# Performance work log

Measured on AMD Instinct MI355X. Metric: run time of the kernel, lower is better.

The kernel has to match this reference:

```python
import jax, jax.numpy as jnp
import numpy as np

DIM = 256
HEADS = 4
B, N = 2, 4096
NEG = -1e9
EPS = 1e-5


def setup_inputs() -> dict:
    key = jax.random.key(0)
    ks = jax.random.split(key, 12)
    s = 0.02
    inp = {
        "x": jax.random.normal(ks[0], (B, N, DIM), dtype=jnp.float32),
        "adj": jax.random.randint(ks[1], (B, N, N), 0, 2, dtype=jnp.int32),
        "Wq": jax.random.normal(ks[2], (DIM, DIM), dtype=jnp.float32) * s,
        "bq": jnp.zeros((DIM,), jnp.float32),
        "Wk": jax.random.normal(ks[3], (DIM, DIM), dtype=jnp.float32) * s,
        "bk": jnp.zeros((DIM,), jnp.float32),
        "Wv": jax.random.normal(ks[4], (DIM, DIM), dtype=jnp.float32) * s,
        "bv": jnp.zeros((DIM,), jnp.float32),
        "Wo": jax.random.normal(ks[5], (DIM, DIM), dtype=jnp.float32) * s,
        "bo": jnp.zeros((DIM,), jnp.float32),
        "gamma": jnp.ones((DIM,), jnp.float32),
        "beta": jnp.zeros((DIM,), jnp.float32),
    }
    return inp


def reference(x, adj, Wq, bq, Wk, bk, Wv, bv, Wo, bo, gamma, beta):
    Bx, Nx, C = x.shape
    H = HEADS
    D = C // H
    scale = D ** (-0.5)
    # torch Linear: y = x @ W.T + b
    def proj(W, b):
        return (x @ W.T + b).reshape(Bx, Nx, H, D).transpose(0, 2, 1, 3)  # [B,H,N,D]
    q = proj(Wq, bq)
    k = proj(Wk, bk)
    v = proj(Wv, bv)
    attn = jnp.einsum("bhnd,bhmd->bhnm", q, k) * scale          # [B,H,N,N]
    attn = jnp.where(adj[:, None, :, :] == 0, NEG, attn)
    attn = jax.nn.softmax(attn, axis=-1)
    # dropout omitted (eval mode / deterministic reference)
    out = jnp.einsum("bhnm,bhmd->bhnd", attn, v)                # [B,H,N,D]
    out = out.transpose(0, 2, 1, 3).reshape(Bx, Nx, C)
    out = out @ Wo.T + bo
    mu = jnp.mean(out, axis=-1, keepdims=True)
    var = jnp.var(out, axis=-1, keepdims=True)
    return (out - mu) * jax.lax.rsqrt(var + EPS) * gamma + beta
```

## Files before the change

### kernel.cpp

```cpp
#include <hip/hip_runtime.h>
#include <stdint.h>

#define CDIM 256
#define HEADS 4
#define HD 64
#define NB 2
#define NN 4096

typedef unsigned short u16;
typedef unsigned long long u64;
typedef __attribute__((ext_vector_type(8))) short short8;
typedef __attribute__((ext_vector_type(4))) float f32x4;

__device__ __forceinline__ void load8f(const float* p, float* f) {
  float4 a = reinterpret_cast<const float4*>(p)[0];
  float4 b = reinterpret_cast<const float4*>(p)[1];
  f[0] = a.x; f[1] = a.y; f[2] = a.z; f[3] = a.w;
  f[4] = b.x; f[5] = b.y; f[6] = b.z; f[7] = b.w;
}

__device__ __forceinline__ u16 f2bf(float f) {
  union { float f; unsigned u; } v; v.f = f;
  return (u16)((v.u + 0x7fffu + ((v.u >> 16) & 1u)) >> 16);
}

__global__ __launch_bounds__(256) void conv_bf16(
    const float* __restrict__ x,
    const float* __restrict__ Wq, const float* __restrict__ Wk,
    const float* __restrict__ Wv, const float* __restrict__ Wo,
    u16* __restrict__ xb, u16* __restrict__ Wqb, u16* __restrict__ Wkb,
    u16* __restrict__ Wvb, u16* __restrict__ Wob) {
  size_t base = ((size_t)blockIdx.x * 256 + threadIdx.x) * 8;
  const float* src;
  u16* dst;
  if (base < 2097152) {
    src = x + base; dst = xb + base;
  } else {
    size_t o = base - 2097152;
    int w = (int)(o >> 16);
    size_t lo = o & 65535;
    if (w == 0)      { src = Wq + lo; dst = Wqb + lo; }
    else if (w == 1) { src = Wk + lo; dst = Wkb + lo; }
    else if (w == 2) { src = Wv + lo; dst = Wvb + lo; }
    else             { src = Wo + lo; dst = Wob + lo; }
  }
  float f[8];
  load8f(src, f);
  short8 h;
#pragma unroll
  for (int i = 0; i < 8; ++i) h[i] = (short)f2bf(f[i]);
  *reinterpret_cast<short8*>(dst) = h;
}

__global__ __launch_bounds__(256) void adj_bits(const int* __restrict__ adj,
                                                u64* __restrict__ bm) {
  const int wave = threadIdx.x >> 6, lane = threadIdx.x & 63;
  const size_t widx = (size_t)blockIdx.x * 4 + wave;
  const size_t base = widx * 512;
#pragma unroll
  for (int it = 0; it < 8; ++it) {
    int a = adj[base + it * 64 + lane];
    u64 m = __ballot(a != 0);
    if (lane == 0) bm[widx * 8 + it] = m;
  }
}

__global__ __launch_bounds__(256) void qkv_gemm(
    const u16* __restrict__ xb,
    const u16* __restrict__ Wqb, const u16* __restrict__ Wkb,
    const u16* __restrict__ Wvb,
    const float* __restrict__ bq, const float* __restrict__ bk,
    const float* __restrict__ bv,
    u16* __restrict__ Qb, u16* __restrict__ Kb, u16* __restrict__ Vtb) {
  const int tid = threadIdx.x, w = tid >> 6, lane = tid & 63;
  const int quad = lane >> 4, l15 = lane & 15;
  const int tok0 = blockIdx.x * 16;
  const int b = tok0 >> 12, nl = tok0 & 4095;
  const int ym = blockIdx.y;

  f32x4 acc[4];
#pragma unroll
  for (int i = 0; i < 4; ++i) acc[i] = (f32x4){0.f, 0.f, 0.f, 0.f};

  if (ym < 2) {
    const u16* Wb = (ym == 0) ? Wqb : Wkb;
    const float* bias = (ym == 0) ? bq : bk;
    const float scale = (ym == 0) ? 0.125f : 1.0f;
    u16* outp = (ym == 0) ? Qb : Kb;
#pragma unroll
    for (int ks = 0; ks < 8; ++ks) {
      short8 af = *reinterpret_cast<const short8*>(
          &xb[(size_t)(tok0 + l15) * 256 + ks * 32 + quad * 8]);
#pragma unroll
      for (int ns = 0; ns < 4; ++ns) {
        short8 bf = *reinterpret_cast<const short8*>(
            &Wb[(size_t)(w * 64 + ns * 16 + l15) * 256 + ks * 32 + quad * 8]);
        acc[ns] = __builtin_amdgcn_mfma_f32_16x16x32_bf16(af, bf, acc[ns], 0, 0, 0);
      }
    }
#pragma unroll
    for (int ns = 0; ns < 4; ++ns) {
      int d = ns * 16 + l15;
      float bb = bias[w * 64 + d];
#pragma unroll
      for (int r = 0; r < 4; ++r) {
        int tok = nl + quad * 4 + r;
        outp[((size_t)(b * HEADS + w) * NN + tok) * HD + d] =
            f2bf((acc[ns][r] + bb) * scale);
      }
    }
  } else {
#pragma unroll
    for (int ks = 0; ks < 8; ++ks) {
      short8 xf = *reinterpret_cast<const short8*>(
          &xb[(size_t)(tok0 + l15) * 256 + ks * 32 + quad * 8]);
#pragma unroll
      for (int ms = 0; ms < 4; ++ms) {
        short8 wf = *reinterpret_cast<const short8*>(
            &Wvb[(size_t)(w * 64 + ms * 16 + l15) * 256 + ks * 32 + quad * 8]);
        acc[ms] = __builtin_amdgcn_mfma_f32_16x16x32_bf16(wf, xf, acc[ms], 0, 0, 0);
      }
    }
#pragma unroll
    for (int ms = 0; ms < 4; ++ms) {
#pragma unroll
      for (int r = 0; r < 4; ++r) {
        int d = ms * 16 + quad * 4 + r;
        float bb = bv[w * 64 + d];
        Vtb[((size_t)((b * HEADS + w) * HD + d)) * NN + nl + l15] =
            f2bf(acc[ms][r] + bb);
      }
    }
  }
}

__global__ __launch_bounds__(256) void attn_mfma(
    const u16* __restrict__ Qb, const u16* __restrict__ Kb,
    const u16* __restrict__ Vtb, const u64* __restrict__ bm,
    u16* __restrict__ Ab) {
  __shared__ u16 Ks[2][64 * 72];
  __shared__ u16 Vs[2][64 * 72];
  __shared__ u16 Ps[4][16 * 72];

  const int tid = threadIdx.x;
  const int wave = tid >> 6, lane = tid & 63;
  const int quad = lane >> 4, l15 = lane & 15;
  const int bh = blockIdx.y, b = bh >> 2, h = bh & 3;
  const int q0 = blockIdx.x * 64 + wave * 16;

  const u16* qr = Qb + ((size_t)bh * NN + q0 + l15) * HD + quad * 8;
  const short8 qf0 = *reinterpret_cast<const short8*>(qr);
  const short8 qf1 = *reinterpret_cast<const short8*>(qr + 32);

  f32x4 Oacc[4];
#pragma unroll
  for (int i = 0; i < 4; ++i) Oacc[i] = (f32x4){0.f, 0.f, 0.f, 0.f};
  float li[4] = {0.f, 0.f, 0.f, 0.f};
  const f32x4 z4 = {0.f, 0.f, 0.f, 0.f};
  u16* Pw = &Ps[wave][0];
  const u64* bmr = bm + ((size_t)b * NN + q0 + quad * 4) * 64;

  const u16* kbase = Kb + (size_t)bh * NN * HD;
  const u16* vbase = Vtb + (size_t)bh * HD * NN;
  const int c0 = tid, c1 = tid + 256;
  const int r0 = c0 >> 3, o0 = (c0 & 7) * 8;
  const int r1 = c1 >> 3, o1 = (c1 & 7) * 8;

  uint4 kreg0, kreg1, vreg0, vreg1;
  kreg0 = *reinterpret_cast<const uint4*>(kbase + (size_t)r0 * HD + o0);
  kreg1 = *reinterpret_cast<const uint4*>(kbase + (size_t)r1 * HD + o1);
  vreg0 = *reinterpret_cast<const uint4*>(vbase + (size_t)r0 * NN + o0);
  vreg1 = *reinterpret_cast<const uint4*>(vbase + (size_t)r1 * NN + o1);
  *reinterpret_cast<uint4*>(&Ks[0][r0 * 72 + o0]) = kreg0;
  *reinterpret_cast<uint4*>(&Ks[0][r1 * 72 + o1]) = kreg1;
  *reinterpret_cast<uint4*>(&Vs[0][r0 * 72 + o0]) = vreg0;
  *reinterpret_cast<uint4*>(&Vs[0][r1 * 72 + o1]) = vreg1;
  __syncthreads();

  for (int mt = 0; mt < 64; ++mt) {
    const int m0 = mt * 64;
    const int buf = mt & 1;
    if (mt + 1 < 64) {
      const int mn = m0 + 64;
      kreg0 = *reinterpret_cast<const uint4*>(kbase + (size_t)(mn + r0) * HD + o0);
      kreg1 = *reinterpret_cast<const uint4*>(kbase + (size_t)(mn + r1) * HD + o1);
      vreg0 = *reinterpret_cast<const uint4*>(vbase + (size_t)r0 * NN + mn + o0);
      vreg1 = *reinterpret_cast<const uint4*>(vbase + (size_t)r1 * NN + mn + o1);
    }

    u64 am[4];
#pragma unroll
    for (int r = 0; r < 4; ++r) am[r] = bmr[r * 64 + mt];

#pragma unroll
    for (int t = 0; t < 4; ++t) {
      const u16* kr = &Ks[buf][(t * 16 + l15) * 72 + quad * 8];
      short8 kf0 = *reinterpret_cast<const short8*>(kr);
      short8 kf1 = *reinterpret_cast<const short8*>(kr + 32);
      f32x4 s = __builtin_amdgcn_mfma_f32_16x16x32_bf16(qf0, kf0, z4, 0, 0, 0);
      s = __builtin_amdgcn_mfma_f32_16x16x32_bf16(qf1, kf1, s, 0, 0, 0);
      const int sh = t * 16 + l15;
#pragma unroll
      for (int r = 0; r < 4; ++r) {
        float p = ((unsigned)(am[r] >> sh) & 1u) ? __expf(s[r]) : 0.f;
        li[r] += p;
        Pw[(quad * 4 + r) * 72 + sh] = f2bf(p);
      }
    }
    __asm__ volatile("s_waitcnt lgkmcnt(0)" ::: "memory");

    const short8 pf0 = *reinterpret_cast<const short8*>(&Pw[l15 * 72 + quad * 8]);
    const short8 pf1 = *reinterpret_cast<const short8*>(&Pw[l15 * 72 + 32 + quad * 8]);
#pragma unroll
    for (int dt = 0; dt < 4; ++dt) {
      const u16* vr = &Vs[buf][(dt * 16 + l15) * 72 + quad * 8];
      short8 vf0 = *reinterpret_cast<const short8*>(vr);
      short8 vf1 = *reinterpret_cast<const short8*>(vr + 32);
      Oacc[dt] = __builtin_amdgcn_mfma_f32_16x16x32_bf16(pf0, vf0, Oacc[dt], 0, 0, 0);
      Oacc[dt] = __builtin_amdgcn_mfma_f32_16x16x32_bf16(pf1, vf1, Oacc[dt], 0, 0, 0);
    }

    if (mt + 1 < 64) {
      const int nb = (mt + 1) & 1;
      *reinterpret_cast<uint4*>(&Ks[nb][r0 * 72 + o0]) = kreg0;
      *reinterpret_cast<uint4*>(&Ks[nb][r1 * 72 + o1]) = kreg1;
      *reinterpret_cast<uint4*>(&Vs[nb][r0 * 72 + o0]) = vreg0;
      *reinterpret_cast<uint4*>(&Vs[nb][r1 * 72 + o1]) = vreg1;
    }
    __syncthreads();
  }

  float inv[4];
#pragma unroll
  for (int r = 0; r < 4; ++r) {
    float lt = li[r];
#pragma unroll
    for (int off = 1; off < 16; off <<= 1) lt += __shfl_xor(lt, off, 64);
    inv[r] = (lt > 0.f) ? (1.f / lt) : 0.f;
  }
#pragma unroll
  for (int r = 0; r < 4; ++r) {
    int tok = q0 + quad * 4 + r;
#pragma unroll
    for (int dt = 0; dt < 4; ++dt) {
      Ab[((size_t)b * NN + tok) * CDIM + h * HD + dt * 16 + l15] =
          f2bf(Oacc[dt][r] * inv[r]);
    }
  }
}

__global__ __launch_bounds__(256) void oproj_ln(
    const u16* __restrict__ Ab, const u16* __restrict__ Wob,
    const float* __restrict__ bo, const float* __restrict__ gamma,
    const float* __restrict__ beta, float* __restrict__ out) {
  __shared__ float ys[16][264];
  const int tid = threadIdx.x, w = tid >> 6, lane = tid & 63;
  const int quad = lane >> 4, l15 = lane & 15;
  const int tok0 = blockIdx.x * 16;

  f32x4 acc[4];
#pragma unroll
  for (int i = 0; i < 4; ++i) acc[i] = (f32x4){0.f, 0.f, 0.f, 0.f};

#pragma unroll
  for (int ks = 0; ks < 8; ++ks) {
    short8 af = *reinterpret_cast<const short8*>(
        &Ab[(size_t)(tok0 + l15) * 256 + ks * 32 + quad * 8]);
#pragma unroll
    for (int ns = 0; ns < 4; ++ns) {
      short8 bf = *reinterpret_cast<const short8*>(
          &Wob[(size_t)(w * 64 + ns * 16 + l15) * 256 + ks * 32 + quad * 8]);
      acc[ns] = __builtin_amdgcn_mfma_f32_16x16x32_bf16(af, bf, acc[ns], 0, 0, 0);
    }
  }

#pragma unroll
  for (int ns = 0; ns < 4; ++ns) {
    int ch = w * 64 + ns * 16 + l15;
    float bb = bo[ch];
#pragma unroll
    for (int r = 0; r < 4; ++r) ys[quad * 4 + r][ch] = acc[ns][r] + bb;
  }
  __syncthreads();

  float g[4], bt[4];
#pragma unroll
  for (int i = 0; i < 4; ++i) {
    g[i] = gamma[lane + i * 64];
    bt[i] = beta[lane + i * 64];
  }
#pragma unroll
  for (int rr = 0; rr < 4; ++rr) {
    int r = w * 4 + rr;
    float v[4], s = 0.f, s2 = 0.f;
#pragma unroll
    for (int i = 0; i < 4; ++i) {
      v[i] = ys[r][lane + i * 64];
      s += v[i];
      s2 = fmaf(v[i], v[i], s2);
    }
#pragma unroll
    for (int off = 32; off > 0; off >>= 1) {
      s += __shfl_xor(s, off, 64);
      s2 += __shfl_xor(s2, off, 64);
    }
    float mu = s * (1.f / 256.f);
    float rs = rsqrtf(s2 * (1.f / 256.f) - mu * mu + 1e-5f);
    float* orow = out + (size_t)(tok0 + r) * 256;
#pragma unroll
    for (int i = 0; i < 4; ++i)
      orow[lane + i * 64] = (v[i] - mu) * rs * g[i] + bt[i];
  }
}

extern "C" void kernel_launch(void* const* d_in, const int* in_sizes, int n_in,
                              void* d_out, int out_size, void* d_ws, size_t ws_size,
                              hipStream_t stream) {
  const float* x     = (const float*)d_in[0];
  const int*   adj   = (const int*)d_in[1];
  const float* Wq    = (const float*)d_in[2];
  const float* bq    = (const float*)d_in[3];
  const float* Wk    = (const float*)d_in[4];
  const float* bk    = (const float*)d_in[5];
  const float* Wv    = (const float*)d_in[6];
  const float* bv    = (const float*)d_in[7];
  const float* Wo    = (const float*)d_in[8];
  const float* bo    = (const float*)d_in[9];
  const float* gamma = (const float*)d_in[10];
  const float* beta  = (const float*)d_in[11];
  float* out = (float*)d_out;

  const size_t PER = (size_t)NB * HEADS * NN * HD;
  u16* xb  = (u16*)d_ws;
  u16* Wqb = xb + 2097152;
  u16* Wkb = Wqb + 65536;
  u16* Wvb = Wkb + 65536;
  u16* Wob = Wvb + 65536;
  u64* bmp = (u64*)(Wob + 65536);
  u16* Qb  = (u16*)(bmp + 524288);
  u16* Kb  = Qb + PER;
  u16* Vtb = Kb + PER;
  u16* Ab  = Vtb + PER;

  const size_t NEED = (size_t)((Ab + PER) - (u16*)d_ws) * sizeof(u16);
  if (ws_size < NEED) return;

  conv_bf16<<<dim3(1152), dim3(256), 0, stream>>>(
      x, Wq, Wk, Wv, Wo, xb, Wqb, Wkb, Wvb, Wob);

  adj_bits<<<dim3(16384), dim3(256), 0, stream>>>(adj, bmp);

  qkv_gemm<<<dim3(512, 3), dim3(256), 0, stream>>>(
      xb, Wqb, Wkb, Wvb, bq, bk, bv, Qb, Kb, Vtb);

  attn_mfma<<<dim3(NN / 64, NB * HEADS), dim3(256), 0, stream>>>(
      Qb, Kb, Vtb, bmp, Ab);

  oproj_ln<<<dim3((NB * NN) / 16), dim3(256), 0, stream>>>(
      Ab, Wob, bo, gamma, beta, out);
}
```

Measured before the change: 360.9 us.

## Split attention keys across two blocks, fuse prep kernels and x conversion

The attention kernel now splits the key range into two halves along a new grid dimension, doubling the block count from 512. Each half writes unnormalized bf16 partial outputs and row sums, which a new combine kernel merges before the output projection and layernorm. The adjacency bitmask and weight conversion are fused into one prep kernel, and x is converted to bf16 inside the QKV GEMM, removing a launch and an intermediate buffer. Q is prescaled by log2(e) so exp2f replaces __expf, and the K/V staging is simplified to a single shared buffer with two barriers per tile, trading overlap and extra partial-output traffic for more parallelism.

```diff
diff --git a/kernel.cpp b/kernel.cpp
--- a/kernel.cpp
+++ b/kernel.cpp
@@ -12,61 +12,67 @@
 typedef __attribute__((ext_vector_type(8))) short short8;
 typedef __attribute__((ext_vector_type(4))) float f32x4;
 
-__device__ __forceinline__ void load8f(const float* p, float* f) {
-  float4 a = reinterpret_cast<const float4*>(p)[0];
-  float4 b = reinterpret_cast<const float4*>(p)[1];
-  f[0] = a.x; f[1] = a.y; f[2] = a.z; f[3] = a.w;
-  f[4] = b.x; f[5] = b.y; f[6] = b.z; f[7] = b.w;
-}
+#define QSCALE 0.1803368801111244f
 
 __device__ __forceinline__ u16 f2bf(float f) {
   union { float f; unsigned u; } v; v.f = f;
   return (u16)((v.u + 0x7fffu + ((v.u >> 16) & 1u)) >> 16);
 }
-
-__global__ __launch_bounds__(256) void conv_bf16(
-    const float* __restrict__ x,
+__device__ __forceinline__ float bf2f(u16 u) {
+  union { unsigned u; float f; } v; v.u = ((unsigned)u) << 16; return v.f;
+}
+
+__global__ __launch_bounds__(256) void prep(
+    const int* __restrict__ adj, u64* __restrict__ bm,
     const float* __restrict__ Wq, const float* __restrict__ Wk,
     const float* __restrict__ Wv, const float* __restrict__ Wo,
-    u16* __restrict__ xb, u16* __restrict__ Wqb, u16* __restrict__ Wkb,
+    u16* __restrict__ Wqb, u16* __restrict__ Wkb,
     u16* __restrict__ Wvb, u16* __restrict__ Wob) {
-  size_t base = ((size_t)blockIdx.x * 256 + threadIdx.x) * 8;
-  const float* src;
-  u16* dst;
-  if (base < 2097152) {
-    src = x + base; dst = xb + base;
+  if (blockIdx.x < 16384) {
+    const int wave = threadIdx.x >> 6, lane = threadIdx.x & 63;
+    const size_t widx = (size_t)blockIdx.x * 4 + wave;
+    const size_t base = widx * 512;
+#pragma unroll
+    for (int it = 0; it < 8; ++it) {
+      int a = adj[base + it * 64 + lane];
+      u64 m = __ballot(a != 0);
+      if (lane == 0) bm[widx * 8 + it] = m;
+    }
   } else {
-    size_t o = base - 2097152;
-    int w = (int)(o >> 16);
-    size_t lo = o & 65535;
+    int bi = blockIdx.x - 16384;
+    size_t base = ((size_t)bi * 256 + threadIdx.x) * 8;
+    int w = (int)(base >> 16);
+    size_t lo = base & 65535;
+    const float* src;
+    u16* dst;
     if (w == 0)      { src = Wq + lo; dst = Wqb + lo; }
     else if (w == 1) { src = Wk + lo; dst = Wkb + lo; }
     else if (w == 2) { src = Wv + lo; dst = Wvb + lo; }
     else             { src = Wo + lo; dst = Wob + lo; }
-  }
-  float f[8];
-  load8f(src, f);
+    float4 a = reinterpret_cast<const float4*>(src)[0];
+    float4 b = reinterpret_cast<const float4*>(src)[1];
+    short8 h;
+    h[0] = (short)f2bf(a.x); h[1] = (short)f2bf(a.y);
+    h[2] = (short)f2bf(a.z); h[3] = (short)f2bf(a.w);
+    h[4] = (short)f2bf(b.x); h[5] = (short)f2bf(b.y);
+    h[6] = (short)f2bf(b.z); h[7] = (short)f2bf(b.w);
+    *reinterpret_cast<short8*>(dst) = h;
+  }
+}
+
+__device__ __forceinline__ short8 fragf32(const float* p) {
+  float4 a = reinterpret_cast<const float4*>(p)[0];
+  float4 b = reinterpret_cast<const float4*>(p)[1];
   short8 h;
-#pragma unroll
-  for (int i = 0; i < 8; ++i) h[i] = (short)f2bf(f[i]);
-  *reinterpret_cast<short8*>(dst) = h;
-}
-
-__global__ __launch_bounds__(256) void adj_bits(const int* __restrict__ adj,
-                                                u64* __restrict__ bm) {
-  const int wave = threadIdx.x >> 6, lane = threadIdx.x & 63;
-  const size_t widx = (size_t)blockIdx.x * 4 + wave;
-  const size_t base = widx * 512;
-#pragma unroll
-  for (int it = 0; it < 8; ++it) {
-    int a = adj[base + it * 64 + lane];
-    u64 m = __ballot(a != 0);
-    if (lane == 0) bm[widx * 8 + it] = m;
-  }
+  h[0] = (short)f2bf(a.x); h[1] = (short)f2bf(a.y);
+  h[2] = (short)f2bf(a.z); h[3] = (short)f2bf(a.w);
+  h[4] = (short)f2bf(b.x); h[5] = (short)f2bf(b.y);
+  h[6] = (short)f2bf(b.z); h[7] = (short)f2bf(b.w);
+  return h;
 }
 
 __global__ __launch_bounds__(256) void qkv_gemm(
-    const u16* __restrict__ xb,
+    const float* __restrict__ x,
     const u16* __restrict__ Wqb, const u16* __restrict__ Wkb,
     const u16* __restrict__ Wvb,
     const float* __restrict__ bq, const float* __restrict__ bk,
@@ -85,12 +91,11 @@
   if (ym < 2) {
     const u16* Wb = (ym == 0) ? Wqb : Wkb;
     const float* bias = (ym == 0) ? bq : bk;
-    const float scale = (ym == 0) ? 0.125f : 1.0f;
+    const float scale = (ym == 0) ? QSCALE : 1.0f;
     u16* outp = (ym == 0) ? Qb : Kb;
 #pragma unroll
     for (int ks = 0; ks < 8; ++ks) {
-      short8 af = *reinterpret_cast<const short8*>(
-          &xb[(size_t)(tok0 + l15) * 256 + ks * 32 + quad * 8]);
+      short8 af = fragf32(x + (size_t)(tok0 + l15) * 256 + ks * 32 + quad * 8);
 #pragma unroll
       for (int ns = 0; ns < 4; ++ns) {
         short8 bf = *reinterpret_cast<const short8*>(
@@ -112,8 +117,7 @@
   } else {
 #pragma unroll
     for (int ks = 0; ks < 8; ++ks) {
-      short8 xf = *reinterpret_cast<const short8*>(
-          &xb[(size_t)(tok0 + l15) * 256 + ks * 32 + quad * 8]);
+      short8 xf = fragf32(x + (size_t)(tok0 + l15) * 256 + ks * 32 + quad * 8);
 #pragma unroll
       for (int ms = 0; ms < 4; ++ms) {
         short8 wf = *reinterpret_cast<const short8*>(
@@ -137,9 +141,9 @@
 __global__ __launch_bounds__(256) void attn_mfma(
     const u16* __restrict__ Qb, const u16* __restrict__ Kb,
     const u16* __restrict__ Vtb, const u64* __restrict__ bm,
-    u16* __restrict__ Ab) {
-  __shared__ u16 Ks[2][64 * 72];
-  __shared__ u16 Vs[2][64 * 72];
+    u16* __restrict__ Opb, float* __restrict__ Lp) {
+  __shared__ u16 Ks[64 * 72];
+  __shared__ u16 Vs[64 * 72];
   __shared__ u16 Ps[4][16 * 72];
 
   const int tid = threadIdx.x;
@@ -147,6 +151,8 @@
   const int quad = lane >> 4, l15 = lane & 15;
   const int bh = blockIdx.y, b = bh >> 2, h = bh & 3;
   const int q0 = blockIdx.x * 64 + wave * 16;
+  const int half = blockIdx.z;
+  const int key0 = half * 2048;
 
   const u16* qr = Qb + ((size_t)bh * NN + q0 + l15) * HD + quad * 8;
   const short8 qf0 = *reinterpret_cast<const short8*>(qr);
@@ -158,34 +164,32 @@
   float li[4] = {0.f, 0.f, 0.f, 0.f};
   const f32x4 z4 = {0.f, 0.f, 0.f, 0.f};
   u16* Pw = &Ps[wave][0];
-  const u64* bmr = bm + ((size_t)b * NN + q0 + quad * 4) * 64;
+  const u64* bmr = bm + ((size_t)b * NN + q0 + quad * 4) * 64 + half * 32;
 
   const u16* kbase = Kb + (size_t)bh * NN * HD;
   const u16* vbase = Vtb + (size_t)bh * HD * NN;
-  const int c0 = tid, c1 = tid + 256;
-  const int r0 = c0 >> 3, o0 = (c0 & 7) * 8;
-  const int r1 = c1 >> 3, o1 = (c1 & 7) * 8;
-
-  uint4 kreg0, kreg1, vreg0, vreg1;
-  kreg0 = *reinterpret_cast<const uint4*>(kbase + (size_t)r0 * HD + o0);
-  kreg1 = *reinterpret_cast<const uint4*>(kbase + (size_t)r1 * HD + o1);
-  vreg0 = *reinterpret_cast<const uint4*>(vbase + (size_t)r0 * NN + o0);
-  vreg1 = *reinterpret_cast<const uint4*>(vbase + (size_t)r1 * NN + o1);
-  *reinterpret_cast<uint4*>(&Ks[0][r0 * 72 + o0]) = kreg0;
-  *reinterpret_cast<uint4*>(&Ks[0][r1 * 72 + o1]) = kreg1;
-  *reinterpret_cast<uint4*>(&Vs[0][r0 * 72 + o0]) = vreg0;
-  *reinterpret_cast<uint4*>(&Vs[0][r1 * 72 + o1]) = vreg1;
-  __syncthreads();
-
-  for (int mt = 0; mt < 64; ++mt) {
-    const int m0 = mt * 64;
-    const int buf = mt & 1;
-    if (mt + 1 < 64) {
-      const int mn = m0 + 64;
-      kreg0 = *reinterpret_cast<const uint4*>(kbase + (size_t)(mn + r0) * HD + o0);
-      kreg1 = *reinterpret_cast<const uint4*>(kbase + (size_t)(mn + r1) * HD + o1);
-      vreg0 = *reinterpret_cast<const uint4*>(vbase + (size_t)r0 * NN + mn + o0);
-      vreg1 = *reinterpret_cast<const uint4*>(vbase + (size_t)r1 * NN + mn + o1);
+  const int rr = tid >> 3, cc8 = (tid & 7) * 8;
+  const int rr2 = rr + 32;
+
+  uint4 k0, k1, v0, v1;
+  k0 = *reinterpret_cast<const uint4*>(kbase + (size_t)(key0 + rr) * HD + cc8);
+  k1 = *reinterpret_cast<const uint4*>(kbase + (size_t)(key0 + rr2) * HD + cc8);
+  v0 = *reinterpret_cast<const uint4*>(vbase + (size_t)rr * NN + key0 + cc8);
+  v1 = *reinterpret_cast<const uint4*>(vbase + (size_t)rr2 * NN + key0 + cc8);
+
+  for (int mt = 0; mt < 32; ++mt) {
+    __syncthreads();
+    *reinterpret_cast<uint4*>(&Ks[rr * 72 + cc8]) = k0;
+    *reinterpret_cast<uint4*>(&Ks[rr2 * 72 + cc8]) = k1;
+    *reinterpret_cast<uint4*>(&Vs[rr * 72 + cc8]) = v0;
+    *reinterpret_cast<uint4*>(&Vs[rr2 * 72 + cc8]) = v1;
+    __syncthreads();
+    if (mt + 1 < 32) {
+      int kb2 = key0 + (mt + 1) * 64;
+      k0 = *reinterpret_cast<const uint4*>(kbase + (size_t)(kb2 + rr) * HD + cc8);
+      k1 = *reinterpret_cast<const uint4*>(kbase + (size_t)(kb2 + rr2) * HD + cc8);
+      v0 = *reinterpret_cast<const uint4*>(vbase + (size_t)rr * NN + kb2 + cc8);
+      v1 = *reinterpret_cast<const uint4*>(vbase + (size_t)rr2 * NN + kb2 + cc8);
     }
 
     u64 am[4];
@@ -194,7 +198,7 @@
 
 #pragma unroll
     for (int t = 0; t < 4; ++t) {
-      const u16* kr = &Ks[buf][(t * 16 + l15) * 72 + quad * 8];
+      const u16* kr = &Ks[(t * 16 + l15) * 72 + quad * 8];
       short8 kf0 = *reinterpret_cast<const short8*>(kr);
       short8 kf1 = *reinterpret_cast<const short8*>(kr + 32);
       f32x4 s = __builtin_amdgcn_mfma_f32_16x16x32_bf16(qf0, kf0, z4, 0, 0, 0);
@@ -202,9 +206,9 @@
       const int sh = t * 16 + l15;
 #pragma unroll
       for (int r = 0; r < 4; ++r) {
-        float p = ((unsigned)(am[r] >> sh) & 1u) ? __expf(s[r]) : 0.f;
+        float p = ((unsigned)(am[r] >> sh) & 1u) ? exp2f(s[r]) : 0.f;
         li[r] += p;
-        Pw[(quad * 4 + r) * 72 + sh] = f2bf(p);
+        Pw[(quad * 4 + r) * 72 + sh] = (u16)(__float_as_uint(p) >> 16);
       }
     }
     __asm__ volatile("s_waitcnt lgkmcnt(0)" ::: "memory");
@@ -213,59 +217,80 @@
     const short8 pf1 = *reinterpret_cast<const short8*>(&Pw[l15 * 72 + 32 + quad * 8]);
 #pragma unroll
     for (int dt = 0; dt < 4; ++dt) {
-      const u16* vr = &Vs[buf][(dt * 16 + l15) * 72 + quad * 8];
+      const u16* vr = &Vs[(dt * 16 + l15) * 72 + quad * 8];
       short8 vf0 = *reinterpret_cast<const short8*>(vr);
       short8 vf1 = *reinterpret_cast<const short8*>(vr + 32);
       Oacc[dt] = __builtin_amdgcn_mfma_f32_16x16x32_bf16(pf0, vf0, Oacc[dt], 0, 0, 0);
       Oacc[dt] = __builtin_amdgcn_mfma_f32_16x16x32_bf16(pf1, vf1, Oacc[dt], 0, 0, 0);
     }
-
-    if (mt + 1 < 64) {
-      const int nb = (mt + 1) & 1;
-      *reinterpret_cast<uint4*>(&Ks[nb][r0 * 72 + o0]) = kreg0;
-      *reinterpret_cast<uint4*>(&Ks[nb][r1 * 72 + o1]) = kreg1;
-      *reinterpret_cast<uint4*>(&Vs[nb][r0 * 72 + o0]) = vreg0;
-      *reinterpret_cast<uint4*>(&Vs[nb][r1 * 72 + o1]) = vreg1;
-    }
-    __syncthreads();
-  }
-
-  float inv[4];
+  }
+
+  u16* ob = Opb + (size_t)(half * NB + b) * NN * CDIM;
 #pragma unroll
   for (int r = 0; r < 4; ++r) {
     float lt = li[r];
 #pragma unroll
     for (int off = 1; off < 16; off <<= 1) lt += __shfl_xor(lt, off, 64);
-    inv[r] = (lt > 0.f) ? (1.f / lt) : 0.f;
-  }
-#pragma unroll
-  for (int r = 0; r < 4; ++r) {
     int tok = q0 + quad * 4 + r;
-#pragma unroll
-    for (int dt = 0; dt < 4; ++dt) {
-      Ab[((size_t)b * NN + tok) * CDIM + h * HD + dt * 16 + l15] =
-          f2bf(Oacc[dt][r] * inv[r]);
-    }
-  }
-}
-
-__global__ __launch_bounds__(256) void oproj_ln(
-    const u16* __restrict__ Ab, const u16* __restrict__ Wob,
-    const float* __restrict__ bo, const float* __restrict__ gamma,
-    const float* __restrict__ beta, float* __restrict__ out) {
+    if (l15 == 0) Lp[((size_t)half * 8 + bh) * NN + tok] = lt;
+#pragma unroll
+    for (int dt = 0; dt < 4; ++dt)
+      ob[(size_t)tok * CDIM + h * HD + dt * 16 + l15] = f2bf(Oacc[dt][r]);
+  }
+}
+
+__global__ __launch_bounds__(256) void comb_oproj(
+    const u16* __restrict__ Opb, const float* __restrict__ Lp,
+    const u16* __restrict__ Wob, const float* __restrict__ bo,
+    const float* __restrict__ gamma, const float* __restrict__ beta,
+    float* __restrict__ out) {
+  __shared__ u16 As[16 * 264];
   __shared__ float ys[16][264];
+  __shared__ float linv[64];
   const int tid = threadIdx.x, w = tid >> 6, lane = tid & 63;
   const int quad = lane >> 4, l15 = lane & 15;
   const int tok0 = blockIdx.x * 16;
+  const int b = tok0 >> 12, nl = tok0 & 4095;
+
+  if (tid < 64) {
+    int tokr = tid >> 2, hh = tid & 3;
+    int bh = b * 4 + hh;
+    int n = nl + tokr;
+    float s = Lp[(size_t)bh * NN + n] + Lp[(size_t)(8 + bh) * NN + n];
+    linv[tokr * 4 + hh] = (s > 0.f) ? (1.f / s) : 0.f;
+  }
+  __syncthreads();
+
+  {
+    int tokr = tid >> 4, ch0 = (tid & 15) * 16;
+    size_t base = ((size_t)b * NN + nl + tokr) * CDIM + ch0;
+    uint4 a0 = *reinterpret_cast<const uint4*>(Opb + base);
+    uint4 a1 = *reinterpret_cast<const uint4*>(Opb + base + 8);
+    uint4 c0 = *reinterpret_cast<const uint4*>(Opb + 2097152 + base);
+    uint4 c1 = *reinterpret_cast<const uint4*>(Opb + 2097152 + base + 8);
+    float inv = linv[tokr * 4 + (ch0 >> 6)];
+    unsigned wa[8] = {a0.x, a0.y, a0.z, a0.w, a1.x, a1.y, a1.z, a1.w};
+    unsigned wb[8] = {c0.x, c0.y, c0.z, c0.w, c1.x, c1.y, c1.z, c1.w};
+    u16 ov[16];
+#pragma unroll
+    for (int i = 0; i < 8; ++i) {
+      float lo = (bf2f((u16)(wa[i] & 0xffffu)) + bf2f((u16)(wb[i] & 0xffffu))) * inv;
+      float hi = (bf2f((u16)(wa[i] >> 16)) + bf2f((u16)(wb[i] >> 16))) * inv;
+      ov[2 * i] = f2bf(lo);
+      ov[2 * i + 1] = f2bf(hi);
+    }
+    u16* dst = &As[tokr * 264 + ch0];
+    *reinterpret_cast<uint4*>(dst) = *reinterpret_cast<uint4*>(ov);
+    *reinterpret_cast<uint4*>(dst + 8) = *reinterpret_cast<uint4*>(ov + 8);
+  }
+  __syncthreads();
 
   f32x4 acc[4];
 #pragma unroll
   for (int i = 0; i < 4; ++i) acc[i] = (f32x4){0.f, 0.f, 0.f, 0.f};
-
 #pragma unroll
   for (int ks = 0; ks < 8; ++ks) {
-    short8 af = *reinterpret_cast<const short8*>(
-        &Ab[(size_t)(tok0 + l15) * 256 + ks * 32 + quad * 8]);
+    short8 af = *reinterpret_cast<const short8*>(&As[l15 * 264 + ks * 32 + quad * 8]);
 #pragma unroll
     for (int ns = 0; ns < 4; ++ns) {
       short8 bf = *reinterpret_cast<const short8*>(
@@ -331,8 +356,7 @@
   float* out = (float*)d_out;
 
   const size_t PER = (size_t)NB * HEADS * NN * HD;
-  u16* xb  = (u16*)d_ws;
-  u16* Wqb = xb + 2097152;
+  u16* Wqb = (u16*)d_ws;
   u16* Wkb = Wqb + 65536;
   u16* Wvb = Wkb + 65536;
   u16* Wob = Wvb + 65536;
@@ -340,22 +364,21 @@
   u16* Qb  = (u16*)(bmp + 524288);
   u16* Kb  = Qb + PER;
   u16* Vtb = Kb + PER;
-  u16* Ab  = Vtb + PER;
-
-  const size_t NEED = (size_t)((Ab + PER) - (u16*)d_ws) * sizeof(u16);
+  u16* Opb = Vtb + PER;
+  float* Lp = (float*)(Opb + 2 * PER);
+
+  const size_t NEED = (size_t)((u16*)(Lp + 65536) - (u16*)d_ws) * sizeof(u16);
   if (ws_size < NEED) return;
 
-  conv_bf16<<<dim3(1152), dim3(256), 0, stream>>>(
-      x, Wq, Wk, Wv, Wo, xb, Wqb, Wkb, Wvb, Wob);
-
-  adj_bits<<<dim3(16384), dim3(256), 0, stream>>>(adj, bmp);
+  prep<<<dim3(16512), dim3(256), 0, stream>>>(
+      adj, bmp, Wq, Wk, Wv, Wo, Wqb, Wkb, Wvb, Wob);
 
   qkv_gemm<<<dim3(512, 3), dim3(256), 0, stream>>>(
-      xb, Wqb, Wkb, Wvb, bq, bk, bv, Qb, Kb, Vtb);
-
-  attn_mfma<<<dim3(NN / 64, NB * HEADS), dim3(256), 0, stream>>>(
-      Qb, Kb, Vtb, bmp, Ab);
-
-  oproj_ln<<<dim3((NB * NN) / 16), dim3(256), 0, stream>>>(
-      Ab, Wob, bo, gamma, beta, out);
-}
+      x, Wqb, Wkb, Wvb, bq, bk, bv, Qb, Kb, Vtb);
+
+  attn_mfma<<<dim3(NN / 64, NB * HEADS, 2), dim3(256), 0, stream>>>(
+      Qb, Kb, Vtb, bmp, Opb, Lp);
+
+  comb_oproj<<<dim3((NB * NN) / 16), dim3(256), 0, stream>>>(
+      Opb, Lp, Wob, bo, gamma, beta, out);
+}
```

Result: faster. 353.1 us (-2.2%).
